# Kernel tuning notes

Hardware: AMD Instinct MI355X
Metric: run time of the kernel (lower is better)

The kernel has to match this reference:

```python
import jax, jax.numpy as jnp
import numpy as np

N_IN, N_HID, N_OUT = 128, 256, 128
B, T = 64, 2048


def setup_inputs() -> dict:
    key = jax.random.key(0)
    ks = jax.random.split(key, 10)
    s_in = 1.0 / np.sqrt(N_IN)
    s_h = 1.0 / np.sqrt(N_HID)
    return {
        "input_signal": jax.random.normal(ks[0], (B, T, N_IN), dtype=jnp.float32),
        "W_in": jax.random.uniform(ks[1], (N_HID, N_IN), jnp.float32, -s_in, s_in),
        "b_in": jax.random.uniform(ks[2], (N_HID,), jnp.float32, -s_in, s_in),
        "W_ih": jax.random.uniform(ks[3], (N_HID, N_HID), jnp.float32, -s_h, s_h),
        "b_ih": jax.random.uniform(ks[4], (N_HID,), jnp.float32, -s_h, s_h),
        "W_hh": jax.random.uniform(ks[5], (N_HID, N_HID), jnp.float32, -s_h, s_h),
        "b_hh": jax.random.uniform(ks[6], (N_HID,), jnp.float32, -s_h, s_h),
        "W_out": jax.random.uniform(ks[7], (N_OUT, N_HID), jnp.float32, -s_h, s_h),
        "b_out": jax.random.uniform(ks[8], (N_OUT,), jnp.float32, -s_h, s_h),
    }


def reference(input_signal, W_in, b_in, W_ih, b_ih, W_hh, b_hh, W_out, b_out):
    # x_t = relu(in_layer(u_t)); h_t = relu(tanh(W_ih x_t + b_ih + W_hh h_{t-1} + b_hh))
    # out_t = out_layer(h_t)
    x = jax.nn.relu(jnp.einsum('bti,hi->bth', input_signal, W_in) + b_in)
    # Precompute the input-to-hidden projection for all timesteps (batched GEMM),
    # leaving only the sequential h @ W_hh recurrence inside the scan.
    pre = jnp.einsum('bth,gh->tbg', x, W_ih) + b_ih  # [T, B, H]
    h0 = jnp.zeros((input_signal.shape[0], W_hh.shape[0]), dtype=input_signal.dtype)

    def step(h, pre_t):
        h_new = jax.nn.relu(jnp.tanh(pre_t + h @ W_hh.T + b_hh))
        return h_new, h_new

    _, hs = jax.lax.scan(step, h0, pre)            # hs: [T, B, H]
    hidden_list = jnp.transpose(hs, (1, 0, 2))     # [B, T, H]
    output_list = jnp.einsum('bth,oh->bto', hidden_list, W_out) + b_out  # [B, T, O]
    return hidden_list, output_list
```

## Files before the change

kernel.cpp:

```cpp
#include <hip/hip_runtime.h>
#include <hip/hip_fp16.h>

typedef _Float16 f16;
typedef __attribute__((ext_vector_type(2))) _Float16 f16x2;
typedef __attribute__((ext_vector_type(8))) _Float16 f16x8;
typedef __attribute__((ext_vector_type(4))) float f32x4;

constexpr int BATCH = 64;
constexpr int TLEN  = 2048;
constexpr int NIN   = 128;
constexpr int NHID  = 256;
constexpr int NOUT  = 128;
constexpr long MROWS = (long)BATCH * TLEN;
constexpr float CSC = 2.8853900817779268f;

__device__ __forceinline__ float exp2f_hw(float x) {
#if __has_builtin(__builtin_amdgcn_exp2f)
  return __builtin_amdgcn_exp2f(x);
#else
  return __expf(x * 0.6931471805599453f);
#endif
}
__device__ __forceinline__ float rcp_hw(float x) {
#if __has_builtin(__builtin_amdgcn_rcpf)
  return __builtin_amdgcn_rcpf(x);
#else
  return 1.0f / x;
#endif
}
__device__ __forceinline__ float fdot2f(unsigned int a, unsigned int b, float c) {
#if __has_builtin(__builtin_amdgcn_fdot2)
  return __builtin_amdgcn_fdot2(__builtin_bit_cast(f16x2, a),
                                __builtin_bit_cast(f16x2, b), c, false);
#else
  f16x2 av = __builtin_bit_cast(f16x2, a);
  f16x2 bv = __builtin_bit_cast(f16x2, b);
  return c + (float)av.x * (float)bv.x + (float)av.y * (float)bv.y;
#endif
}
template<int CTRL>
__device__ __forceinline__ float dpp_xor(float x) {
  int r = __builtin_amdgcn_update_dpp(0, __builtin_bit_cast(int, x),
                                      CTRL, 0xF, 0xF, true);
  return __builtin_bit_cast(float, r);
}
__device__ __forceinline__ float xor32_partner(float x, int lane) {
#if __has_builtin(__builtin_amdgcn_permlane32_swap)
  auto r = __builtin_amdgcn_permlane32_swap(
      __builtin_bit_cast(unsigned int, x), __builtin_bit_cast(unsigned int, x),
      false, false);
  unsigned int pv = (lane < 32) ? r[1] : r[0];
  return __builtin_bit_cast(float, pv);
#else
  return __builtin_bit_cast(float, __builtin_amdgcn_ds_bpermute(
      ((lane ^ 32) << 2), __builtin_bit_cast(int, x)));
#endif
}
__device__ __forceinline__ void barrier_lds() {
  asm volatile("s_waitcnt lgkmcnt(0)" ::: "memory");
  __builtin_amdgcn_s_barrier();
  asm volatile("" ::: "memory");
}

__global__ void cvt_weights(const float* __restrict__ Win, const float* __restrict__ Wih,
                            const float* __restrict__ Whh, const float* __restrict__ Wout,
                            f16* __restrict__ dst) {
  int i = blockIdx.x * blockDim.x + threadIdx.x;
  if (i < 32768) {
    float v = Win[i]; f16 h = (f16)v;
    dst[i] = h; dst[32768 + i] = (f16)(v - (float)h);
  } else if (i < 98304) {
    int j = i - 32768; float v = Wih[j]; f16 h = (f16)v;
    dst[65536 + j] = h; dst[131072 + j] = (f16)(v - (float)h);
  } else if (i < 163840) {
    int j = i - 98304; dst[196608 + j] = (f16)(CSC * Whh[j]);
  } else if (i < 196608) {
    int j = i - 163840; dst[262144 + j] = (f16)Wout[j];
  }
}

constexpr int BM = 64, BN = 64, BK = 64;

template<int MODE>
__global__ __launch_bounds__(256)
void gemm_kernel(const void* __restrict__ Ap, const void* __restrict__ Ap2,
                 const f16* __restrict__ Bh_, const f16* __restrict__ Bl_,
                 const float* __restrict__ bias, const float* __restrict__ bias2,
                 void* __restrict__ Cp, void* __restrict__ Cp2,
                 int K, int N) {
  __shared__ __align__(16) f16 Ah[BM][BK + 8];
  __shared__ __align__(16) f16 Al[BM][BK + 8];
  __shared__ __align__(16) f16 Bh[BN][BK + 8];
  __shared__ __align__(16) f16 Bl[BN][BK + 8];

  const int tid  = threadIdx.x;
  const int lane = tid & 63;
  const int wid  = tid >> 6;
  const int wm = wid >> 1, wn = wid & 1;
  const long row0 = (long)blockIdx.x * BM;
  const int  col0 = blockIdx.y * BN;
  const int r  = tid >> 2;
  const int cc = (tid & 3) * 16;

  f32x4 acc[2][2] = {};

  for (int k0 = 0; k0 < K; k0 += BK) {
    if constexpr (MODE == 1) {
      const float* src = (const float*)Ap + (row0 + r) * (long)K + k0 + cc;
      #pragma unroll
      for (int q = 0; q < 4; ++q) {
        float4 v = ((const float4*)src)[q];
        f16 h0 = (f16)v.x, h1 = (f16)v.y, h2 = (f16)v.z, h3 = (f16)v.w;
        Ah[r][cc + 4*q + 0] = h0;  Al[r][cc + 4*q + 0] = (f16)(v.x - (float)h0);
        Ah[r][cc + 4*q + 1] = h1;  Al[r][cc + 4*q + 1] = (f16)(v.y - (float)h1);
        Ah[r][cc + 4*q + 2] = h2;  Al[r][cc + 4*q + 2] = (f16)(v.z - (float)h2);
        Ah[r][cc + 4*q + 3] = h3;  Al[r][cc + 4*q + 3] = (f16)(v.w - (float)h3);
      }
    } else if constexpr (MODE == 2) {
      const f16* sh = (const f16*)Ap  + (row0 + r) * (long)K + k0 + cc;
      const f16* sl = (const f16*)Ap2 + (row0 + r) * (long)K + k0 + cc;
      *(uint4*)&Ah[r][cc]     = *(const uint4*)sh;
      *(uint4*)&Ah[r][cc + 8] = *(const uint4*)(sh + 8);
      *(uint4*)&Al[r][cc]     = *(const uint4*)sl;
      *(uint4*)&Al[r][cc + 8] = *(const uint4*)(sl + 8);
    } else {
      const f16* sh = (const f16*)Ap + (row0 + r) * (long)K + k0 + cc;
      *(uint4*)&Ah[r][cc]     = *(const uint4*)sh;
      *(uint4*)&Ah[r][cc + 8] = *(const uint4*)(sh + 8);
    }
    {
      const f16* sh = Bh_ + (col0 + r) * (long)K + k0 + cc;
      *(uint4*)&Bh[r][cc]     = *(const uint4*)sh;
      *(uint4*)&Bh[r][cc + 8] = *(const uint4*)(sh + 8);
      if constexpr (MODE != 3) {
        const f16* sl = Bl_ + (col0 + r) * (long)K + k0 + cc;
        *(uint4*)&Bl[r][cc]     = *(const uint4*)sl;
        *(uint4*)&Bl[r][cc + 8] = *(const uint4*)(sl + 8);
      }
    }
    __syncthreads();

    #pragma unroll
    for (int ks = 0; ks < BK / 32; ++ks) {
      const int ko = ks * 32 + (lane >> 4) * 8;
      const int ra = wm * 32 + (lane & 15);
      const int rb = wn * 32 + (lane & 15);
      f16x8 a0 = *(const f16x8*)&Ah[ra][ko];
      f16x8 a1 = *(const f16x8*)&Ah[ra + 16][ko];
      f16x8 b0 = *(const f16x8*)&Bh[rb][ko];
      f16x8 b1 = *(const f16x8*)&Bh[rb + 16][ko];
      acc[0][0] = __builtin_amdgcn_mfma_f32_16x16x32_f16(a0, b0, acc[0][0], 0, 0, 0);
      acc[0][1] = __builtin_amdgcn_mfma_f32_16x16x32_f16(a0, b1, acc[0][1], 0, 0, 0);
      acc[1][0] = __builtin_amdgcn_mfma_f32_16x16x32_f16(a1, b0, acc[1][0], 0, 0, 0);
      acc[1][1] = __builtin_amdgcn_mfma_f32_16x16x32_f16(a1, b1, acc[1][1], 0, 0, 0);
      if constexpr (MODE != 3) {
        f16x8 la0 = *(const f16x8*)&Al[ra][ko];
        f16x8 la1 = *(const f16x8*)&Al[ra + 16][ko];
        f16x8 lb0 = *(const f16x8*)&Bl[rb][ko];
        f16x8 lb1 = *(const f16x8*)&Bl[rb + 16][ko];
        acc[0][0] = __builtin_amdgcn_mfma_f32_16x16x32_f16(a0, lb0, acc[0][0], 0, 0, 0);
        acc[0][0] = __builtin_amdgcn_mfma_f32_16x16x32_f16(la0, b0, acc[0][0], 0, 0, 0);
        acc[0][1] = __builtin_amdgcn_mfma_f32_16x16x32_f16(a0, lb1, acc[0][1], 0, 0, 0);
        acc[0][1] = __builtin_amdgcn_mfma_f32_16x16x32_f16(la0, b1, acc[0][1], 0, 0, 0);
        acc[1][0] = __builtin_amdgcn_mfma_f32_16x16x32_f16(a1, lb0, acc[1][0], 0, 0, 0);
        acc[1][0] = __builtin_amdgcn_mfma_f32_16x16x32_f16(la1, b0, acc[1][0], 0, 0, 0);
        acc[1][1] = __builtin_amdgcn_mfma_f32_16x16x32_f16(a1, lb1, acc[1][1], 0, 0, 0);
        acc[1][1] = __builtin_amdgcn_mfma_f32_16x16x32_f16(la1, b1, acc[1][1], 0, 0, 0);
      }
    }
    __syncthreads();
  }

  #pragma unroll
  for (int mi = 0; mi < 2; ++mi)
    #pragma unroll
    for (int ni = 0; ni < 2; ++ni)
      #pragma unroll
      for (int q = 0; q < 4; ++q) {
        long row = row0 + wm * 32 + mi * 16 + (lane >> 4) * 4 + q;
        int  col = col0 + wn * 32 + ni * 16 + (lane & 15);
        if constexpr (MODE == 1) {
          float v = fmaxf(acc[mi][ni][q] + bias[col], 0.0f);
          f16 h = (f16)v;
          ((f16*)Cp )[row * (long)N + col] = h;
          ((f16*)Cp2)[row * (long)N + col] = (f16)(v - (float)h);
        } else if constexpr (MODE == 2) {
          float v = (acc[mi][ni][q] + bias[col] + bias2[col]) * CSC;
          ((float*)Cp)[row * (long)N + col] = v;
        } else {
          ((float*)Cp)[row * (long)N + col] = acc[mi][ni][q] + bias[col];
        }
      }
}

#define STEP(K, SRC, DST, P) do {                                            \
  unsigned int hs[16];                                                       \
  _Pragma("unroll")                                                          \
  for (int q = 0; q < 4; ++q) {                                              \
    uint4 v = *(const uint4*)((SRC) + roff[q]);                              \
    hs[4*q+0] = v.x; hs[4*q+1] = v.y; hs[4*q+2] = v.z; hs[4*q+3] = v.w;      \
  }                                                                          \
  float sA0 = 0.f, sA1 = 0.f, sA2 = 0.f, sA3 = 0.f;                          \
  float sB0 = 0.f, sB1 = 0.f, sB2 = 0.f, sB3 = 0.f;                          \
  _Pragma("unroll")                                                          \
  for (int m = 0; m < 8; ++m) {                                              \
    sA0 = fdot2f(wr[0][m], hs[m], sA0);                                      \
    sA1 = fdot2f(wr[1][m], hs[m], sA1);                                      \
    sA2 = fdot2f(wr[2][m], hs[m], sA2);                                      \
    sA3 = fdot2f(wr[3][m], hs[m], sA3);                                      \
  }                                                                          \
  _Pragma("unroll")                                                          \
  for (int m = 8; m < 16; ++m) {                                             \
    sB0 = fdot2f(wr[0][m], hs[m], sB0);                                      \
    sB1 = fdot2f(wr[1][m], hs[m], sB1);                                      \
    sB2 = fdot2f(wr[2][m], hs[m], sB2);                                      \
    sB3 = fdot2f(wr[3][m], hs[m], sB3);                                      \
  }                                                                          \
  float sv0 = sA0 + sB0, sv1 = sA1 + sB1;                                    \
  float sv2 = sA2 + sB2, sv3 = sA3 + sB3;                                    \
                               \
  float k0 = s0 ? sv1 : sv0, d0 = s0 ? sv0 : sv1;                            \
  float k1 = s0 ? sv3 : sv2, d1 = s0 ? sv2 : sv3;                            \
  float t0 = k0 + dpp_xor<0xB1>(d0);                                         \
  float t1 = k1 + dpp_xor<0xB1>(d1);                                         \
                              \
  float rk = s1 ? t1 : t0, rs = s1 ? t0 : t1;                                \
  float z2 = rk + dpp_xor<0x4E>(rs);                                         \
                                                \
  float z  = z2 + xor32_partner(z2, lane) + (P);                             \
  float ee = exp2f_hw(z);                                                    \
  float hv = fmaxf(fmaf(-2.0f, rcp_hw(ee + 1.0f), 1.0f), 0.0f);              \
  f16 hf = (f16)hv;                                                          \
  if (lane < 32) *(f16*)((DST) + wo) = hf;        \
  else           hp[(K) * 256] = hf;            \
} while (0)

__global__ __launch_bounds__(512, 1)
void rec_kernel(const float* __restrict__ pre, const f16* __restrict__ W2,
                f16* __restrict__ h16) {
  const int b    = blockIdx.x;
  const int tid  = threadIdx.x;
  const int lane = tid & 63;
  const int w    = tid >> 6;
  const int jj   = (lane & 3) | ((lane >> 5) << 2);
  const int s0   = lane & 1;
  const int s1   = (lane >> 1) & 1;
  const int G8   = ((lane >> 2) & 7) | (w << 3);
  const int g    = 32 * w + (lane & 31);

  __shared__ __align__(16) char hb[2][512];

  unsigned int wr[4][16];
  #pragma unroll
  for (int i = 0; i < 4; ++i)
    #pragma unroll
    for (int q = 0; q < 4; ++q) {
      int c = (q + jj) & 3;
      uint4 v = *(const uint4*)(W2 + (size_t)(4 * G8 + i) * 256 + 32 * jj + 8 * c);
      wr[i][4*q+0] = v.x; wr[i][4*q+1] = v.y; wr[i][4*q+2] = v.z; wr[i][4*q+3] = v.w;
    }
  if (tid < 128) ((unsigned int*)&hb[0][0])[tid] = 0u;
  __syncthreads();

  int roff[4];
  #pragma unroll
  for (int q = 0; q < 4; ++q) roff[q] = 64 * jj + 16 * ((q + jj) & 3);
  const int wo = 2 * g;

  const float* pp  = pre + (size_t)b * TLEN * 256 + g;
  f16*         hp  = h16 + (size_t)b * TLEN * 256 + g;
  const float* ppf = pp + 1024;

  float p0 = pp[0];
  float p1 = pp[256];
  float p2 = pp[512];
  float p3 = pp[768];

  const char* hb0 = &hb[0][0];
  char*       hb1 = &hb[1][0];

  #pragma unroll 1
  for (int t = 0; t < TLEN; t += 4) {
    float n0 = ppf[0];
    float n1 = ppf[256];
    float n2 = ppf[512];
    float n3 = ppf[768];
    STEP(0, hb0, hb1, p0);
    barrier_lds();
    STEP(1, hb1, (char*)hb0, p1);
    barrier_lds();
    STEP(2, hb0, hb1, p2);
    barrier_lds();
    STEP(3, hb1, (char*)hb0, p3);
    barrier_lds();
    p0 = n0; p1 = n1; p2 = n2; p3 = n3;
    ppf += 1024;
    hp  += 1024;
  }
}

__global__ __launch_bounds__(256)
void cvt_h(const f16* __restrict__ src, float* __restrict__ dst, long n) {
  long i0 = ((long)blockIdx.x * 256 + threadIdx.x) * 8;
  long stride = (long)gridDim.x * 256 * 8;
  for (long i = i0; i < n; i += stride) {
    f16x8 v = *(const f16x8*)(src + i);
    float4 a = {(float)v[0], (float)v[1], (float)v[2], (float)v[3]};
    float4 bq = {(float)v[4], (float)v[5], (float)v[6], (float)v[7]};
    *(float4*)(dst + i) = a;
    *(float4*)(dst + i + 4) = bq;
  }
}

extern "C" void kernel_launch(void* const* d_in, const int* in_sizes, int n_in,
                              void* d_out, int out_size, void* d_ws, size_t ws_size,
                              hipStream_t stream) {
  const float* input = (const float*)d_in[0];
  const float* W_in  = (const float*)d_in[1];
  const float* b_in  = (const float*)d_in[2];
  const float* W_ih  = (const float*)d_in[3];
  const float* b_ih  = (const float*)d_in[4];
  const float* W_hh  = (const float*)d_in[5];
  const float* b_hh  = (const float*)d_in[6];
  const float* W_out = (const float*)d_in[7];
  const float* b_out = (const float*)d_in[8];

  float* hidden = (float*)d_out;
  float* outp   = (float*)d_out + MROWS * NHID;

  char* ws = (char*)d_ws;
  const size_t xh_off  = 0;
  const size_t xl_off  = (size_t)MROWS * NHID * 2;
  const size_t pre_off = xl_off * 2;
  const size_t w_off   = pre_off + (size_t)MROWS * NHID * 4;
  const size_t need    = w_off + 294912ull * 2;
  if (ws_size < need) return;

  f16*   x_hi  = (f16*)(ws + xh_off);
  f16*   x_lo  = (f16*)(ws + xl_off);
  float* pre   = (float*)(ws + pre_off);
  f16*   wbase = (f16*)(ws + w_off);
  f16 *WinH = wbase,           *WinL = wbase + 32768;
  f16 *WihH = wbase + 65536,   *WihL = wbase + 131072;
  f16 *Whh16 = wbase + 196608, *Wout16 = wbase + 262144;
  f16* h16 = x_hi;

  cvt_weights<<<768, 256, 0, stream>>>(W_in, W_ih, W_hh, W_out, wbase);

  dim3 g12((unsigned)(MROWS / BM), NHID / BN);
  gemm_kernel<1><<<g12, 256, 0, stream>>>(input, nullptr, WinH, WinL, b_in, nullptr,
                                          x_hi, x_lo, NIN, NHID);
  gemm_kernel<2><<<g12, 256, 0, stream>>>(x_hi, x_lo, WihH, WihL, b_ih, b_hh,
                                          pre, nullptr, NHID, NHID);

  rec_kernel<<<BATCH, 512, 0, stream>>>(pre, Whh16, h16);

  cvt_h<<<2048, 256, 0, stream>>>(h16, hidden, MROWS * NHID);

  dim3 g3((unsigned)(MROWS / BM), NOUT / BN);
  gemm_kernel<3><<<g3, 256, 0, stream>>>(h16, nullptr, Wout16, nullptr, b_out, nullptr,
                                         outp, nullptr, NHID, NOUT);
}
```

Baseline: 1.194 ms.

## Split recurrence dot products across 1024 threads with extra cross-lane reduction

The recurrent kernel now runs 1024 threads per batch row instead of 512. Each lane holds half as many W_hh weights and computes a 16-element-pair dot product. An additional permlane16 reduction stage combines the partial sums. The aim is to shorten the per-step serial dot-product latency on the critical recurrence path, at the cost of more cross-lane shuffles and a larger barrier across 16 waves each step.

```diff
diff --git a/kernel.cpp b/kernel.cpp
--- a/kernel.cpp
+++ b/kernel.cpp
@@ -5,6 +5,7 @@
 typedef __attribute__((ext_vector_type(2))) _Float16 f16x2;
 typedef __attribute__((ext_vector_type(8))) _Float16 f16x8;
 typedef __attribute__((ext_vector_type(4))) float f32x4;
+typedef __attribute__((ext_vector_type(8))) unsigned int u32x8;
 
 constexpr int BATCH = 64;
 constexpr int TLEN  = 2048;
@@ -54,6 +55,18 @@
 #else
   return __builtin_bit_cast(float, __builtin_amdgcn_ds_bpermute(
       ((lane ^ 32) << 2), __builtin_bit_cast(int, x)));
+#endif
+}
+__device__ __forceinline__ float xor16_partner(float x, int lane) {
+#if __has_builtin(__builtin_amdgcn_permlane16_swap)
+  auto r = __builtin_amdgcn_permlane16_swap(
+      __builtin_bit_cast(unsigned int, x), __builtin_bit_cast(unsigned int, x),
+      false, false);
+  unsigned int pv = ((lane & 16) == 0) ? r[1] : r[0];
+  return __builtin_bit_cast(float, pv);
+#else
+  return __builtin_bit_cast(float, __builtin_amdgcn_ds_bpermute(
+      ((lane ^ 16) << 2), __builtin_bit_cast(int, x)));
 #endif
 }
 __device__ __forceinline__ void barrier_lds() {
@@ -194,78 +207,74 @@
 }
 
 #define STEP(K, SRC, DST, P) do {                                            \
-  unsigned int hs[16];                                                       \
-  _Pragma("unroll")                                                          \
-  for (int q = 0; q < 4; ++q) {                                              \
-    uint4 v = *(const uint4*)((SRC) + roff[q]);                              \
-    hs[4*q+0] = v.x; hs[4*q+1] = v.y; hs[4*q+2] = v.z; hs[4*q+3] = v.w;      \
-  }                                                                          \
-  float sA0 = 0.f, sA1 = 0.f, sA2 = 0.f, sA3 = 0.f;                          \
-  float sB0 = 0.f, sB1 = 0.f, sB2 = 0.f, sB3 = 0.f;                          \
+  uint4 va = *(const uint4*)((SRC) + roff0);                                 \
+  uint4 vb = *(const uint4*)((SRC) + roff1);                                 \
+  unsigned int hs[8] = {va.x, va.y, va.z, va.w, vb.x, vb.y, vb.z, vb.w};     \
+  float sv0 = 0.f, sv1 = 0.f, sv2 = 0.f, sv3 = 0.f;                          \
   _Pragma("unroll")                                                          \
   for (int m = 0; m < 8; ++m) {                                              \
-    sA0 = fdot2f(wr[0][m], hs[m], sA0);                                      \
-    sA1 = fdot2f(wr[1][m], hs[m], sA1);                                      \
-    sA2 = fdot2f(wr[2][m], hs[m], sA2);                                      \
-    sA3 = fdot2f(wr[3][m], hs[m], sA3);                                      \
+    sv0 = fdot2f(wv0[m], hs[m], sv0);                                        \
+    sv1 = fdot2f(wv1[m], hs[m], sv1);                                        \
+    sv2 = fdot2f(wv2[m], hs[m], sv2);                                        \
+    sv3 = fdot2f(wv3[m], hs[m], sv3);                                        \
   }                                                                          \
-  _Pragma("unroll")                                                          \
-  for (int m = 8; m < 16; ++m) {                                             \
-    sB0 = fdot2f(wr[0][m], hs[m], sB0);                                      \
-    sB1 = fdot2f(wr[1][m], hs[m], sB1);                                      \
-    sB2 = fdot2f(wr[2][m], hs[m], sB2);                                      \
-    sB3 = fdot2f(wr[3][m], hs[m], sB3);                                      \
-  }                                                                          \
-  float sv0 = sA0 + sB0, sv1 = sA1 + sB1;                                    \
-  float sv2 = sA2 + sB2, sv3 = sA3 + sB3;                                    \
-                               \
+          \
   float k0 = s0 ? sv1 : sv0, d0 = s0 ? sv0 : sv1;                            \
   float k1 = s0 ? sv3 : sv2, d1 = s0 ? sv2 : sv3;                            \
   float t0 = k0 + dpp_xor<0xB1>(d0);                                         \
   float t1 = k1 + dpp_xor<0xB1>(d1);                                         \
-                              \
+                            \
   float rk = s1 ? t1 : t0, rs = s1 ? t0 : t1;                                \
   float z2 = rk + dpp_xor<0x4E>(rs);                                         \
-                                                \
-  float z  = z2 + xor32_partner(z2, lane) + (P);                             \
+                                 \
+  float z3 = z2 + xor16_partner(z2, lane);                                   \
+  float z  = z3 + xor32_partner(z3, lane) + (P);                             \
   float ee = exp2f_hw(z);                                                    \
   float hv = fmaxf(fmaf(-2.0f, rcp_hw(ee + 1.0f), 1.0f), 0.0f);              \
   f16 hf = (f16)hv;                                                          \
-  if (lane < 32) *(f16*)((DST) + wo) = hf;        \
-  else           hp[(K) * 256] = hf;            \
+  int wsel = lane & 48;                                                      \
+  if (wsel == 0)       *(f16*)((DST) + wo) = hf;             \
+  else if (wsel == 16) hp[(K) * 256] = hf;                   \
 } while (0)
 
-__global__ __launch_bounds__(512, 1)
-void rec_kernel(const float* __restrict__ pre, const f16* __restrict__ W2,
-                f16* __restrict__ h16) {
+#define LOADW(dst, i) do {                                                   \
+  _Pragma("unroll")                                                          \
+  for (int c = 0; c < 2; ++c) {                                              \
+    int ccw = (c + rot) & 1;                                                 \
+    uint4 v = *(const uint4*)(W2 + (size_t)(4 * G + (i)) * 256               \
+                              + 16 * jj + 8 * ccw);                          \
+    dst[4*c+0] = v.x; dst[4*c+1] = v.y; dst[4*c+2] = v.z; dst[4*c+3] = v.w;  \
+  }                                                                          \
+} while (0)
+
+__global__ __launch_bounds__(1024)
+void rec_kernel(const float* __restrict__ pre, const f16* W2, f16* h16) {
   const int b    = blockIdx.x;
   const int tid  = threadIdx.x;
   const int lane = tid & 63;
   const int w    = tid >> 6;
-  const int jj   = (lane & 3) | ((lane >> 5) << 2);
+  const int jj   = (lane & 3) | (((lane >> 4) & 1) << 2) | ((lane >> 5) << 3);
   const int s0   = lane & 1;
   const int s1   = (lane >> 1) & 1;
-  const int G8   = ((lane >> 2) & 7) | (w << 3);
-  const int g    = 32 * w + (lane & 31);
+  const int G    = ((lane >> 2) & 3) | (w << 2);
+  const int g    = 4 * G + 2 * s1 + s0;
+  const int rot  = (jj + (jj >> 2)) & 1;
 
   __shared__ __align__(16) char hb[2][512];
 
-  unsigned int wr[4][16];
-  #pragma unroll
-  for (int i = 0; i < 4; ++i)
-    #pragma unroll
-    for (int q = 0; q < 4; ++q) {
-      int c = (q + jj) & 3;
-      uint4 v = *(const uint4*)(W2 + (size_t)(4 * G8 + i) * 256 + 32 * jj + 8 * c);
-      wr[i][4*q+0] = v.x; wr[i][4*q+1] = v.y; wr[i][4*q+2] = v.z; wr[i][4*q+3] = v.w;
-    }
+  u32x8 wv0, wv1, wv2, wv3;
+  LOADW(wv0, 0);
+  LOADW(wv1, 1);
+  LOADW(wv2, 2);
+  LOADW(wv3, 3);
+  asm volatile("" : "+v"(wv0), "+v"(wv1), "+v"(wv2), "+v"(wv3));
+
   if (tid < 128) ((unsigned int*)&hb[0][0])[tid] = 0u;
   __syncthreads();
 
-  int roff[4];
-  #pragma unroll
-  for (int q = 0; q < 4; ++q) roff[q] = 64 * jj + 16 * ((q + jj) & 3);
-  const int wo = 2 * g;
+  const int roff0 = 32 * jj + 16 * rot;
+  const int roff1 = 32 * jj + 16 * ((1 + rot) & 1);
+  const int wo    = 2 * g;
 
   const float* pp  = pre + (size_t)b * TLEN * 256 + g;
   f16*         hp  = h16 + (size_t)b * TLEN * 256 + g;
@@ -353,7 +362,7 @@
   gemm_kernel<2><<<g12, 256, 0, stream>>>(x_hi, x_lo, WihH, WihL, b_ih, b_hh,
                                           pre, nullptr, NHID, NHID);
 
-  rec_kernel<<<BATCH, 512, 0, stream>>>(pre, Whh16, h16);
+  rec_kernel<<<BATCH, 1024, 0, stream>>>(pre, Whh16, h16);
 
   cvt_h<<<2048, 256, 0, stream>>>(h16, hidden, MROWS * NHID);
 
```

Result: slower. 1.402 ms (+17.4%).
